# Optimization experiments

Hardware: AMD Instinct MI355X
Metric: run time of the kernel (lower is better)

## Reference

```python
import jax, jax.numpy as jnp
import numpy as np

N_NODES = 100000
N_EDGES = 1600000
D = 32


def setup_inputs() -> dict:
    key = jax.random.key(0)
    k1, k2, k3, k4, k5, k6, k7 = jax.random.split(key, 7)
    x = jax.random.normal(k1, (N_NODES, D), dtype=jnp.float32)
    edge_index = jax.random.randint(k2, (2, N_EDGES), 0, N_NODES, dtype=jnp.int64)
    edge_weight = jax.random.uniform(k3, (N_EDGES,), dtype=jnp.float32)
    s = 1.0 / np.sqrt(D)
    W1 = jax.random.uniform(k4, (D, D), jnp.float32, -s, s)
    b1 = jax.random.uniform(k5, (D,), jnp.float32, -s, s)
    W2 = jax.random.uniform(k6, (D, D), jnp.float32, -s, s)
    b2 = jax.random.uniform(k7, (D,), jnp.float32, -s, s)
    return {"x": x, "edge_index": edge_index, "edge_weight": edge_weight,
            "W1": W1, "b1": b1, "W2": W2, "b2": b2}


def reference(x, edge_index, edge_weight, W1, b1, W2, b2):
    N = x.shape[0]
    src, dst = edge_index[0], edge_index[1]
    # gcn_norm with improved=True: self-loops get fill value 2.0
    loops = jnp.arange(N, dtype=edge_index.dtype)
    src_a = jnp.concatenate([src, loops])
    dst_a = jnp.concatenate([dst, loops])
    w_a = jnp.concatenate([edge_weight, jnp.full((N,), 2.0, x.dtype)])
    deg = jax.ops.segment_sum(w_a, dst_a, num_segments=N)          # [N]
    dinv = jnp.where(deg > 0, jax.lax.rsqrt(deg), 0.0)             # deg^-1/2, inf->0
    norm = dinv[src_a] * w_a * dinv[dst_a]                          # [E+N]

    def gcn_conv(h, W, b):
        h = h @ W                                                   # [N,D] dense transform
        msg = h[src_a] * norm[:, None]                              # gather + normalize [E+N,D]
        return jax.ops.segment_sum(msg, dst_a, num_segments=N) + b  # scatter-add + bias

    h = jax.nn.relu(gcn_conv(x, W1, b1))
    h = jax.nn.relu(gcn_conv(h, W2, b2))
    # F.dropout treated as identity (deterministic inference reference)
    return h
```

## Files before the change

kernel.cpp:

```cpp
#include <hip/hip_runtime.h>

#define D       32
#define BS      256
#define CBLK    500
#define CBLKP   500
#define BSH     7
#define BNODES  128
#define MAXBUCK 1024
#define MAX_EPT 13
#define ECAP    4096
#define POISON_BASE ((int)0xAAAAAAAAu)

__device__ inline unsigned bf16pack2(float a, float b) {
    unsigned ua = __float_as_uint(a);
    unsigned ub = __float_as_uint(b);
    ua = (ua + 0x7FFFu + ((ua >> 16) & 1)) >> 16;
    ub = (ub + 0x7FFFu + ((ub >> 16) & 1)) >> 16;
    return ua | (ub << 16);
}
__device__ inline uint2 bf16pack4(float4 v) {
    return make_uint2(bf16pack2(v.x, v.y), bf16pack2(v.z, v.w));
}
__device__ inline float4 bf16unpack4(uint2 h) {
    return make_float4(__uint_as_float(h.x << 16),
                       __uint_as_float(h.x & 0xFFFF0000u),
                       __uint_as_float(h.y << 16),
                       __uint_as_float(h.y & 0xFFFF0000u));
}

__global__ void k_localsort_gemm(const int* __restrict__ dst, const int* __restrict__ src,
                                 const float* __restrict__ w, int* __restrict__ bc,
                                 int* __restrict__ locoff, int2* __restrict__ staged,
                                 int E, int EPB, int NBUCK, int NBUCKP,
                                 const float* __restrict__ X, const float* __restrict__ Wm,
                                 uint2* __restrict__ H, int n) {
    __shared__ int    bins[MAXBUCK];
    __shared__ int    sscan[BS];
    __shared__ int    carry;
    __shared__ float4 Ws[D * 8];
    int t = threadIdx.x;

    if ((int)blockIdx.x >= CBLK) {
        for (int i = t; i < D * 8; i += BS) Ws[i] = ((const float4*)Wm)[i];
        __syncthreads();
        int gid  = (blockIdx.x - CBLK) * BS + t;
        int node = gid >> 3;
        int q    = gid & 7;
        if (node >= n) return;
        float4 xv  = ((const float4*)X)[node * 8 + q];
        float4 acc = make_float4(0.f, 0.f, 0.f, 0.f);
#pragma unroll
        for (int k = 0; k < D; ++k) {
            float comp = (k & 3) == 0 ? xv.x : (k & 3) == 1 ? xv.y
                       : (k & 3) == 2 ? xv.z : xv.w;
            float  xk = __shfl(comp, k >> 2, 8);
            float4 wr = Ws[k * 8 + q];
            acc.x += xk * wr.x; acc.y += xk * wr.y;
            acc.z += xk * wr.z; acc.w += xk * wr.w;
        }
        H[node * 8 + q] = bf16pack4(acc);
        return;
    }

    int blk = blockIdx.x;
    int beg = blk * EPB;
    int end = min(E, beg + EPB);
    for (int i = t; i < NBUCK; i += BS) bins[i] = 0;
    __syncthreads();

    int stash[MAX_EPT];
#pragma unroll
    for (int i = 0; i < MAX_EPT; ++i) {
        int e = beg + i * BS + t;
        stash[i] = -1;
        if (e < end) {
            int dv = dst[e];
            int b  = dv >> BSH;
            int r  = atomicAdd(&bins[b], 1);
            stash[i] = (b << 19) | ((dv & (BNODES - 1)) << 12) | r;
        }
    }
    __syncthreads();
    for (int i = t; i < NBUCK; i += BS) bc[blk * NBUCKP + i] = bins[i];
    __syncthreads();
    if (t == 0) carry = 0;
    __syncthreads();
    for (int base = 0; base < NBUCK; base += BS) {
        int idx = base + t;
        int v = (idx < NBUCK) ? bins[idx] : 0;
        sscan[t] = v;
        __syncthreads();
        for (int off = 1; off < BS; off <<= 1) {
            int u = (t >= off) ? sscan[t - off] : 0;
            __syncthreads();
            sscan[t] += u;
            __syncthreads();
        }
        if (idx < NBUCK) bins[idx] = carry + sscan[t] - v;
        __syncthreads();
        if (t == 0) carry += sscan[BS - 1];
        __syncthreads();
    }
    for (int i = t; i < NBUCK; i += BS) locoff[blk * NBUCKP + i] = bins[i];
    __syncthreads();

    int2* myslice = staged + (size_t)blk * EPB;
#pragma unroll
    for (int i = 0; i < MAX_EPT; ++i) {
        if (stash[i] >= 0) {
            int e     = beg + i * BS + t;
            int b     = stash[i] >> 19;
            int local = (stash[i] >> 12) & (BNODES - 1);
            int r     = stash[i] & 0xFFF;
            int pos   = bins[b] + r;
            myslice[pos] = make_int2(src[e] | (local << 17), __float_as_int(w[e]));
        }
    }
}

__global__ void k_trans(const int* __restrict__ bc, const int* __restrict__ locoff,
                        int* __restrict__ bcT, int* __restrict__ locoffT,
                        int NBUCK, int NBUCKP) {
    __shared__ int tile[32][33];
    const int* in  = (blockIdx.z == 0) ? bc  : locoff;
    int*       out = (blockIdx.z == 0) ? bcT : locoffT;
    int c0 = blockIdx.x * 32;
    int r0 = blockIdx.y * 32;
    int tx = threadIdx.x & 31, ty = threadIdx.x >> 5;
    for (int dy = ty; dy < 32; dy += 8) {
        int r = r0 + dy, c = c0 + tx;
        tile[dy][tx] = (r < CBLK && c < NBUCK) ? in[r * NBUCKP + c] : 0;
    }
    __syncthreads();
    for (int dy = ty; dy < 32; dy += 8) {
        int c = c0 + dy, r = r0 + tx;
        if (c < NBUCK && r < CBLK) out[c * CBLKP + r] = tile[tx][dy];
    }
}

__global__ void k_btot(const int* __restrict__ bcT, int* __restrict__ btot, int NBUCK) {
    int gid = blockIdx.x * BS + threadIdx.x;
    int b = gid >> 3, c = gid & 7;
    if (b >= NBUCK) return;
    int s = 0;
    for (int k = c; k < CBLK; k += 8) s += bcT[b * CBLKP + k];
    s += __shfl_xor(s, 4, 8);
    s += __shfl_xor(s, 2, 8);
    s += __shfl_xor(s, 1, 8);
    if (c == 0) btot[b] = s;
}

__global__ void k_scanB(const int* __restrict__ asum, int* __restrict__ aex, int m) {
    __shared__ int s[BS];
    __shared__ int carry;
    int t = threadIdx.x;
    if (t == 0) carry = 0;
    __syncthreads();
    for (int base = 0; base < m; base += BS) {
        int i = base + t;
        int v = (i < m) ? asum[i] : 0;
        s[t] = v;
        __syncthreads();
        for (int off = 1; off < BS; off <<= 1) {
            int u = (t >= off) ? s[t - off] : 0;
            __syncthreads();
            s[t] += u;
            __syncthreads();
        }
        if (i < m) aex[i] = carry + s[t] - v;
        __syncthreads();
        if (t == BS - 1) carry += s[BS - 1];
        __syncthreads();
    }
}

__global__ void k_merge(const int* __restrict__ bcT, const int* __restrict__ locoffT,
                        const int* __restrict__ boff, const int2* __restrict__ staged,
                        int2* __restrict__ emeta, int* __restrict__ rowptr,
                        float* __restrict__ dinv, uint2* __restrict__ H,
                        int N, int E, int NBUCK, int EPB) {
    __shared__ int2  ebuf[ECAP];
    __shared__ int   runoff[CBLK];
    __shared__ int   lrun[CBLK];
    __shared__ int   sscan[BS];
    __shared__ int   carry;
    __shared__ int   ihist[BNODES];
    __shared__ float fdeg[BNODES];
    __shared__ int   cursor[BNODES];
    __shared__ float sdinv[BNODES];
    __shared__ int   wsum;
    int b = blockIdx.x, t = threadIdx.x;

    for (int k = t; k < CBLK; k += BS) {
        runoff[k] = bcT[b * CBLKP + k];
        lrun[k]   = locoffT[b * CBLKP + k];
    }
    if (t < BNODES) { ihist[t] = 0; fdeg[t] = 0.0f; }
    if (t == 0) carry = 0;
    __syncthreads();
    for (int base = 0; base < CBLK; base += BS) {
        int idx = base + t;
        int v = (idx < CBLK) ? runoff[idx] : 0;
        sscan[t] = v;
        __syncthreads();
        for (int off = 1; off < BS; off <<= 1) {
            int u = (t >= off) ? sscan[t - off] : 0;
            __syncthreads();
            sscan[t] += u;
            __syncthreads();
        }
        if (idx < CBLK) runoff[idx] = carry + sscan[t] - v;
        __syncthreads();
        if (t == 0) carry += sscan[BS - 1];
        __syncthreads();
    }
    int total  = carry;
    int bstart = boff[b];
    bool fits  = total <= ECAP;

    for (int k = t; k < CBLK; k += BS) {
        int gs = runoff[k];
        int ge = (k + 1 < CBLK) ? runoff[k + 1] : total;
        const int2* run = staged + (size_t)k * EPB + lrun[k];
        for (int j = 0; j < ge - gs; ++j) {
            int2 v = run[j];
            int local = (v.x >> 17) & (BNODES - 1);
            atomicAdd(&ihist[local], 1);
            atomicAdd(&fdeg[local], __int_as_float(v.y));
            if (fits) ebuf[gs + j] = v;
        }
    }
    __syncthreads();
    int v128 = 0, incl = 0;
    if (t < BNODES) {
        v128 = ihist[t];
        incl = v128;
#pragma unroll
        for (int off = 1; off < 64; off <<= 1) {
            int u = __shfl_up(incl, off, 64);
            if ((t & 63) >= off) incl += u;
        }
    }
    if (t == 63) wsum = incl;
    __syncthreads();
    if (t < BNODES) {
        if (t >= 64) incl += wsum;
        int excl = incl - v128;
        int node = b * BNODES + t;
        float di = rsqrtf(2.0f + fdeg[t]);
        if (node < N) {
            rowptr[node] = bstart + excl;
            dinv[node]   = di;
        }
        sdinv[t]  = di;
        cursor[t] = excl;
    }
    if (b == NBUCK - 1 && t == 0) rowptr[N] = E;
    __syncthreads();
    {
        int base_node = b * BNODES;
        for (int i = t; i < BNODES * 8; i += BS) {
            int row  = i >> 3;
            int node = base_node + row;
            if (node < N) {
                float di = sdinv[row];
                size_t off = (size_t)node * 8 + (i & 7);
                float4 f = bf16unpack4(H[off]);
                f.x *= di; f.y *= di; f.z *= di; f.w *= di;
                H[off] = bf16pack4(f);
            }
        }
    }
    __syncthreads();
    for (int k = t; k < CBLK; k += BS) {
        int gs = runoff[k];
        int ge = (k + 1 < CBLK) ? runoff[k + 1] : total;
        const int2* run = staged + (size_t)k * EPB + lrun[k];
        for (int j = 0; j < ge - gs; ++j) {
            int2 v = fits ? ebuf[gs + j] : run[j];
            int local = (v.x >> 17) & (BNODES - 1);
            int r = atomicAdd(&cursor[local], 1);
            emeta[bstart + r] = make_int2(v.x & 0x1FFFF, v.y);
        }
    }
}

template <bool FUSE_GEMM>
__global__ void k_agg(const int* __restrict__ rowptr, const int2* __restrict__ emeta,
                      const uint4* __restrict__ Hs, const float* __restrict__ dinv,
                      const float* __restrict__ b, const float* __restrict__ W2,
                      void* __restrict__ outv, int n) {
    __shared__ float4 Ws[D * 8];
    int tid = threadIdx.x;
    if (FUSE_GEMM) {
        for (int i = tid; i < D * 8; i += BS) Ws[i] = ((const float4*)W2)[i];
        __syncthreads();
    }

    int gid  = blockIdx.x * BS + tid;
    int node = gid >> 2;
    int q    = gid & 3;
    if (node >= n) return;

    float  di  = dinv[node];
    float4 bq0 = ((const float4*)b)[q * 2];
    float4 bq1 = ((const float4*)b)[q * 2 + 1];
    uint4  h0  = Hs[node * 4 + q];
    float4 a0  = bf16unpack4(make_uint2(h0.x, h0.y));
    float4 a1  = bf16unpack4(make_uint2(h0.z, h0.w));
    float4 acc0 = make_float4(2.f * a0.x, 2.f * a0.y, 2.f * a0.z, 2.f * a0.w);
    float4 acc1 = make_float4(2.f * a1.x, 2.f * a1.y, 2.f * a1.z, 2.f * a1.w);

    int beg  = rowptr[node];
    int end  = rowptr[node + 1];
    int full = beg + ((end - beg) & ~7);

    for (int i0 = beg; i0 < full; i0 += 8) {
        int2 em0 = emeta[i0 + q];
        int2 em1 = emeta[i0 + 4 + q];
        float nm0 = __int_as_float(em0.y);
        float nm1 = __int_as_float(em1.y);
#pragma unroll
        for (int j = 0; j < 4; ++j) {
            int   s  = __shfl(em0.x, j, 4);
            float nm = __shfl(nm0, j, 4);
            uint4 hv = Hs[s * 4 + q];
            float4 f0 = bf16unpack4(make_uint2(hv.x, hv.y));
            float4 f1 = bf16unpack4(make_uint2(hv.z, hv.w));
            acc0.x += nm * f0.x; acc0.y += nm * f0.y; acc0.z += nm * f0.z; acc0.w += nm * f0.w;
            acc1.x += nm * f1.x; acc1.y += nm * f1.y; acc1.z += nm * f1.z; acc1.w += nm * f1.w;
        }
#pragma unroll
        for (int j = 0; j < 4; ++j) {
            int   s  = __shfl(em1.x, j, 4);
            float nm = __shfl(nm1, j, 4);
            uint4 hv = Hs[s * 4 + q];
            float4 f0 = bf16unpack4(make_uint2(hv.x, hv.y));
            float4 f1 = bf16unpack4(make_uint2(hv.z, hv.w));
            acc0.x += nm * f0.x; acc0.y += nm * f0.y; acc0.z += nm * f0.z; acc0.w += nm * f0.w;
            acc1.x += nm * f1.x; acc1.y += nm * f1.y; acc1.z += nm * f1.z; acc1.w += nm * f1.w;
        }
    }
    if (full < end) {
        int idx0 = full + q;
        int idx1 = full + 4 + q;
        int2 em0 = (idx0 < end) ? emeta[idx0] : make_int2(0, 0);
        int2 em1 = (idx1 < end) ? emeta[idx1] : make_int2(0, 0);
        float nm0 = (idx0 < end) ? __int_as_float(em0.y) : 0.0f;
        float nm1 = (idx1 < end) ? __int_as_float(em1.y) : 0.0f;
        int rem = end - full;
        int r0 = rem < 4 ? rem : 4;
        for (int j = 0; j < r0; ++j) {
            int   s  = __shfl(em0.x, j, 4);
            float nm = __shfl(nm0, j, 4);
            uint4 hv = Hs[s * 4 + q];
            float4 f0 = bf16unpack4(make_uint2(hv.x, hv.y));
            float4 f1 = bf16unpack4(make_uint2(hv.z, hv.w));
            acc0.x += nm * f0.x; acc0.y += nm * f0.y; acc0.z += nm * f0.z; acc0.w += nm * f0.w;
            acc1.x += nm * f1.x; acc1.y += nm * f1.y; acc1.z += nm * f1.z; acc1.w += nm * f1.w;
        }
        for (int j = 0; j < rem - 4; ++j) {
            int   s  = __shfl(em1.x, j, 4);
            float nm = __shfl(nm1, j, 4);
            uint4 hv = Hs[s * 4 + q];
            float4 f0 = bf16unpack4(make_uint2(hv.x, hv.y));
            float4 f1 = bf16unpack4(make_uint2(hv.z, hv.w));
            acc0.x += nm * f0.x; acc0.y += nm * f0.y; acc0.z += nm * f0.z; acc0.w += nm * f0.w;
            acc1.x += nm * f1.x; acc1.y += nm * f1.y; acc1.z += nm * f1.z; acc1.w += nm * f1.w;
        }
    }
    acc0.x = fmaxf(di * acc0.x + bq0.x, 0.f);
    acc0.y = fmaxf(di * acc0.y + bq0.y, 0.f);
    acc0.z = fmaxf(di * acc0.z + bq0.z, 0.f);
    acc0.w = fmaxf(di * acc0.w + bq0.w, 0.f);
    acc1.x = fmaxf(di * acc1.x + bq1.x, 0.f);
    acc1.y = fmaxf(di * acc1.y + bq1.y, 0.f);
    acc1.z = fmaxf(di * acc1.z + bq1.z, 0.f);
    acc1.w = fmaxf(di * acc1.w + bq1.w, 0.f);

    if (FUSE_GEMM) {
        float4 o0 = make_float4(0.f, 0.f, 0.f, 0.f);
        float4 o1 = make_float4(0.f, 0.f, 0.f, 0.f);
#pragma unroll
        for (int k = 0; k < D; ++k) {
            int sel = k & 7;
            float comp = sel == 0 ? acc0.x : sel == 1 ? acc0.y : sel == 2 ? acc0.z
                       : sel == 3 ? acc0.w : sel == 4 ? acc1.x : sel == 5 ? acc1.y
                       : sel == 6 ? acc1.z : acc1.w;
            float  hk = __shfl(comp, k >> 3, 4);
            float4 w0 = Ws[k * 8 + q * 2];
            float4 w1 = Ws[k * 8 + q * 2 + 1];
            o0.x += hk * w0.x; o0.y += hk * w0.y; o0.z += hk * w0.z; o0.w += hk * w0.w;
            o1.x += hk * w1.x; o1.y += hk * w1.y; o1.z += hk * w1.z; o1.w += hk * w1.w;
        }
        o0.x *= di; o0.y *= di; o0.z *= di; o0.w *= di;
        o1.x *= di; o1.y *= di; o1.z *= di; o1.w *= di;
        ((uint4*)outv)[node * 4 + q] =
            make_uint4(bf16pack2(o0.x, o0.y), bf16pack2(o0.z, o0.w),
                       bf16pack2(o1.x, o1.y), bf16pack2(o1.z, o1.w));
    } else {
        ((float4*)outv)[node * 8 + q * 2]     = acc0;
        ((float4*)outv)[node * 8 + q * 2 + 1] = acc1;
    }
}

__global__ void k_hist_gemm(const int4* __restrict__ dst4, int* __restrict__ cnt,
                            int4* __restrict__ rank4, int E4,
                            const float* __restrict__ X, const float* __restrict__ W,
                            uint2* __restrict__ H, int n, int gE4) {
    __shared__ float4 Ws[D * 8];
    int tid = threadIdx.x;
    if ((int)blockIdx.x < gE4) {
        int i = blockIdx.x * BS + tid;
        if (i >= E4) return;
        int4 d = dst4[i];
        int4 r;
        r.x = atomicAdd(&cnt[d.x], 1) - POISON_BASE;
        r.y = atomicAdd(&cnt[d.y], 1) - POISON_BASE;
        r.z = atomicAdd(&cnt[d.z], 1) - POISON_BASE;
        r.w = atomicAdd(&cnt[d.w], 1) - POISON_BASE;
        rank4[i] = r;
        return;
    }
    for (int i = tid; i < D * 8; i += BS) Ws[i] = ((const float4*)W)[i];
    __syncthreads();
    int gid  = (blockIdx.x - gE4) * BS + tid;
    int node = gid >> 3;
    int q    = gid & 7;
    if (node >= n) return;
    float4 xv  = ((const float4*)X)[node * 8 + q];
    float4 acc = make_float4(0.f, 0.f, 0.f, 0.f);
#pragma unroll
    for (int k = 0; k < D; ++k) {
        float comp = (k & 3) == 0 ? xv.x : (k & 3) == 1 ? xv.y
                   : (k & 3) == 2 ? xv.z : xv.w;
        float  xk = __shfl(comp, k >> 2, 8);
        float4 wr = Ws[k * 8 + q];
        acc.x += xk * wr.x; acc.y += xk * wr.y;
        acc.z += xk * wr.z; acc.w += xk * wr.w;
    }
    H[node * 8 + q] = bf16pack4(acc);
}

__global__ void k_scan1(const int* __restrict__ cnt, int* __restrict__ bsum, int n) {
    __shared__ int s[BS];
    int t = threadIdx.x, i = blockIdx.x * BS + t;
    s[t] = (i < n) ? (cnt[i] - POISON_BASE) : 0;
    __syncthreads();
    for (int off = BS / 2; off > 0; off >>= 1) {
        if (t < off) s[t] += s[t + off];
        __syncthreads();
    }
    if (t == 0) bsum[blockIdx.x] = s[0];
}

__global__ void k_scan23(const int* __restrict__ cnt, const int* __restrict__ bsum,
                         int* __restrict__ rowptr, int n) {
    __shared__ int red[BS];
    __shared__ int s[BS];
    int t = threadIdx.x, i = blockIdx.x * BS + t;
    int pacc = 0;
    for (int k = t; k < (int)blockIdx.x; k += BS) pacc += bsum[k];
    red[t] = pacc;
    __syncthreads();
    for (int off = BS / 2; off > 0; off >>= 1) {
        if (t < off) red[t] += red[t + off];
        __syncthreads();
    }
    int bpre = red[0];
    int v = (i < n) ? (cnt[i] - POISON_BASE) : 0;
    s[t] = v;
    __syncthreads();
    for (int off = 1; off < BS; off <<= 1) {
        int u = (t >= off) ? s[t - off] : 0;
        __syncthreads();
        s[t] += u;
        __syncthreads();
    }
    if (i < n) {
        int excl = bpre + s[t] - v;
        rowptr[i] = excl;
        if (i == n - 1) rowptr[n] = excl + v;
    }
}

__global__ void k_reorder(const int4* __restrict__ src4, const int4* __restrict__ dst4,
                          const float4* __restrict__ w4, const int4* __restrict__ rank4,
                          const int* __restrict__ rowptr, int2* __restrict__ emeta, int E4) {
    int i = blockIdx.x * blockDim.x + threadIdx.x;
    if (i >= E4) return;
    int4   s = src4[i];
    int4   d = dst4[i];
    float4 w = w4[i];
    int4   r = rank4[i];
    emeta[rowptr[d.x] + r.x] = make_int2(s.x, __float_as_int(w.x));
    emeta[rowptr[d.y] + r.y] = make_int2(s.y, __float_as_int(w.y));
    emeta[rowptr[d.z] + r.z] = make_int2(s.z, __float_as_int(w.z));
    emeta[rowptr[d.w] + r.w] = make_int2(s.w, __float_as_int(w.w));
}

__global__ void k_degscaleF(const int* __restrict__ rowptr, const int2* __restrict__ emeta,
                            float* __restrict__ dinv, uint2* __restrict__ H, int n) {
    int gid  = blockIdx.x * blockDim.x + threadIdx.x;
    int node = gid >> 3;
    int c    = gid & 7;
    if (node >= n) return;
    int beg = rowptr[node], end = rowptr[node + 1];
    float sum = 0.0f;
    for (int idx = beg + c; idx < end; idx += 8)
        sum += __int_as_float(emeta[idx].y);
    sum += __shfl_xor(sum, 4, 8);
    sum += __shfl_xor(sum, 2, 8);
    sum += __shfl_xor(sum, 1, 8);
    float di = rsqrtf(2.0f + sum);
    if (c == 0) dinv[node] = di;
    di = __shfl(di, 0, 8);
    size_t off = (size_t)node * 8 + c;
    float4 f = bf16unpack4(H[off]);
    f.x *= di; f.y *= di; f.z *= di; f.w *= di;
    H[off] = bf16pack4(f);
}

extern "C" void kernel_launch(void* const* d_in, const int* in_sizes, int n_in,
                              void* d_out, int out_size, void* d_ws, size_t ws_size,
                              hipStream_t stream) {
    const float* x   = (const float*)d_in[0];
    const int*   ei  = (const int*)d_in[1];
    const float* w   = (const float*)d_in[2];
    const float* W1  = (const float*)d_in[3];
    const float* b1  = (const float*)d_in[4];
    const float* W2  = (const float*)d_in[5];
    const float* b2  = (const float*)d_in[6];
    float*       out = (float*)d_out;

    const int N = in_sizes[0] / D;
    const int E = in_sizes[2];
    const int* src = ei;
    const int* dst = ei + E;

    const int NBUCK  = (N + BNODES - 1) / BNODES;
    const int NBUCKP = (NBUCK + 3) & ~3;
    const int EPB    = (E + CBLK - 1) / CBLK;
    const int NB     = (N + BS - 1) / BS;
    const int E4     = E / 4;
    const int gE4    = (E4 + BS - 1) / BS;
    const int gN8    = (N * 8 + BS - 1) / BS;
    const int gN4    = (N * 4 + BS - 1) / BS;

    char*  base    = (char*)d_ws;
    int2*  emeta   = (int2*)base;
    uint2* ht      = (uint2*)(base + (size_t)E * 8);
    uint2* ht2     = ht + (size_t)N * 8;
    float* dinv    = (float*)(ht2 + (size_t)N * 8);
    int*   rowptr  = (int*)(dinv + N);
    int2*  staged  = (int2*)(rowptr + ((N + 4) & ~3));
    int*   bc      = (int*)(staged + E);
    int*   locoff  = bc + (size_t)CBLK * NBUCKP;
    int*   bcT     = locoff + (size_t)CBLK * NBUCKP;
    int*   locoffT = bcT + (size_t)NBUCK * CBLKP;
    int*   btot    = locoffT + (size_t)NBUCK * CBLKP;
    int*   boff    = btot + NBUCKP;
    size_t need    = (size_t)((char*)(boff + NBUCKP) - base);

    bool main_ok = (ws_size >= need) && (NBUCK <= MAXBUCK) && (N < (1 << 17)) &&
                   ((EPB + BS - 1) / BS <= MAX_EPT) && (EPB <= 4096) && (N % 4 == 0);

    if (main_ok) {
        k_localsort_gemm<<<CBLK + gN8, BS, 0, stream>>>(dst, src, w, bc, locoff, staged,
                                                        E, EPB, NBUCK, NBUCKP, x, W1, ht, N);
        dim3 tg((NBUCK + 31) / 32, (CBLK + 31) / 32, 2);
        k_trans<<<tg, BS, 0, stream>>>(bc, locoff, bcT, locoffT, NBUCK, NBUCKP);
        k_btot <<<(NBUCK * 8 + BS - 1) / BS, BS, 0, stream>>>(bcT, btot, NBUCK);
        k_scanB<<<1, BS, 0, stream>>>(btot, boff, NBUCK);
        k_merge<<<NBUCK, BS, 0, stream>>>(bcT, locoffT, boff, staged, emeta, rowptr, dinv,
                                          ht, N, E, NBUCK, EPB);
        k_agg<true ><<<gN4, BS, 0, stream>>>(rowptr, emeta, (const uint4*)ht,  dinv, b1, W2, ht2, N);
        k_agg<false><<<gN4, BS, 0, stream>>>(rowptr, emeta, (const uint4*)ht2, dinv, b2, nullptr, out, N);
    } else {
        int* cnt  = (int*)staged;
        int* rank = cnt + N;
        int* bsum = rank + E;
        k_hist_gemm<<<gE4 + gN8, BS, 0, stream>>>((const int4*)dst, cnt, (int4*)rank, E4,
                                                  x, W1, ht, N, gE4);
        k_scan1 <<<NB, BS, 0, stream>>>(cnt, bsum, N);
        k_scan23<<<NB, BS, 0, stream>>>(cnt, bsum, rowptr, N);
        k_reorder<<<(E4 + BS - 1) / BS, BS, 0, stream>>>((const int4*)src, (const int4*)dst,
                                                         (const float4*)w, (const int4*)rank,
                                                         rowptr, emeta, E4);
        k_degscaleF<<<gN8, BS, 0, stream>>>(rowptr, emeta, dinv, ht, N);
        k_agg<true ><<<gN4, BS, 0, stream>>>(rowptr, emeta, (const uint4*)ht,  dinv, b1, W2, ht2, N);
        k_agg<false><<<gN4, BS, 0, stream>>>(rowptr, emeta, (const uint4*)ht2, dinv, b2, nullptr, out, N);
    }
}
```

Baseline: 208.5 us.

## Fold bucket totals into transpose, compute offsets in merge, cache edge loads

Bucket totals are now accumulated with atomics inside the transpose kernel. Each merge block computes its own exclusive prefix by reducing the totals of all preceding buckets, which removes two kernel launches (k_btot and the single-block k_scanB). The local sort also loads src and w once into registers during the first pass, so the scatter pass no longer re-reads them from global memory. The cost is a memset launch, redundant O(NBUCK) reductions in every merge block, and more registers per thread in the local sort.

```diff
diff --git a/kernel.cpp b/kernel.cpp
--- a/kernel.cpp
+++ b/kernel.cpp
@@ -68,7 +68,9 @@
     for (int i = t; i < NBUCK; i += BS) bins[i] = 0;
     __syncthreads();
 
-    int stash[MAX_EPT];
+    int   stash[MAX_EPT];
+    int   ssrc[MAX_EPT];
+    float swv[MAX_EPT];
 #pragma unroll
     for (int i = 0; i < MAX_EPT; ++i) {
         int e = beg + i * BS + t;
@@ -77,7 +79,9 @@
             int dv = dst[e];
             int b  = dv >> BSH;
             int r  = atomicAdd(&bins[b], 1);
-            stash[i] = (b << 19) | ((dv & (BNODES - 1)) << 12) | r;
+            stash[i] = (b << 12) | r;
+            ssrc[i]  = src[e] | ((dv & (BNODES - 1)) << 17);
+            swv[i]   = w[e];
         }
     }
     __syncthreads();
@@ -108,19 +112,17 @@
 #pragma unroll
     for (int i = 0; i < MAX_EPT; ++i) {
         if (stash[i] >= 0) {
-            int e     = beg + i * BS + t;
-            int b     = stash[i] >> 19;
-            int local = (stash[i] >> 12) & (BNODES - 1);
-            int r     = stash[i] & 0xFFF;
-            int pos   = bins[b] + r;
-            myslice[pos] = make_int2(src[e] | (local << 17), __float_as_int(w[e]));
+            int b   = stash[i] >> 12;
+            int r   = stash[i] & 0xFFF;
+            int pos = bins[b] + r;
+            myslice[pos] = make_int2(ssrc[i], __float_as_int(swv[i]));
         }
     }
 }
 
 __global__ void k_trans(const int* __restrict__ bc, const int* __restrict__ locoff,
                         int* __restrict__ bcT, int* __restrict__ locoffT,
-                        int NBUCK, int NBUCKP) {
+                        int* __restrict__ btot, int NBUCK, int NBUCKP) {
     __shared__ int tile[32][33];
     const int* in  = (blockIdx.z == 0) ? bc  : locoff;
     int*       out = (blockIdx.z == 0) ? bcT : locoffT;
@@ -136,46 +138,16 @@
         int c = c0 + dy, r = r0 + tx;
         if (c < NBUCK && r < CBLK) out[c * CBLKP + r] = tile[tx][dy];
     }
-}
-
-__global__ void k_btot(const int* __restrict__ bcT, int* __restrict__ btot, int NBUCK) {
-    int gid = blockIdx.x * BS + threadIdx.x;
-    int b = gid >> 3, c = gid & 7;
-    if (b >= NBUCK) return;
-    int s = 0;
-    for (int k = c; k < CBLK; k += 8) s += bcT[b * CBLKP + k];
-    s += __shfl_xor(s, 4, 8);
-    s += __shfl_xor(s, 2, 8);
-    s += __shfl_xor(s, 1, 8);
-    if (c == 0) btot[b] = s;
-}
-
-__global__ void k_scanB(const int* __restrict__ asum, int* __restrict__ aex, int m) {
-    __shared__ int s[BS];
-    __shared__ int carry;
-    int t = threadIdx.x;
-    if (t == 0) carry = 0;
-    __syncthreads();
-    for (int base = 0; base < m; base += BS) {
-        int i = base + t;
-        int v = (i < m) ? asum[i] : 0;
-        s[t] = v;
-        __syncthreads();
-        for (int off = 1; off < BS; off <<= 1) {
-            int u = (t >= off) ? s[t - off] : 0;
-            __syncthreads();
-            s[t] += u;
-            __syncthreads();
-        }
-        if (i < m) aex[i] = carry + s[t] - v;
-        __syncthreads();
-        if (t == BS - 1) carry += s[BS - 1];
-        __syncthreads();
+    if (blockIdx.z == 0 && ty == 0 && c0 + tx < NBUCK) {
+        int s = 0;
+#pragma unroll
+        for (int dy = 0; dy < 32; ++dy) s += tile[dy][tx];
+        if (s) atomicAdd(&btot[c0 + tx], s);
     }
 }
 
 __global__ void k_merge(const int* __restrict__ bcT, const int* __restrict__ locoffT,
-                        const int* __restrict__ boff, const int2* __restrict__ staged,
+                        const int* __restrict__ btot, const int2* __restrict__ staged,
                         int2* __restrict__ emeta, int* __restrict__ rowptr,
                         float* __restrict__ dinv, uint2* __restrict__ H,
                         int N, int E, int NBUCK, int EPB) {
@@ -189,7 +161,22 @@
     __shared__ int   cursor[BNODES];
     __shared__ float sdinv[BNODES];
     __shared__ int   wsum;
+    __shared__ int   bstart_s;
     int b = blockIdx.x, t = threadIdx.x;
+
+    {
+        int pacc = 0;
+        for (int k = t; k < b; k += BS) pacc += btot[k];
+        sscan[t] = pacc;
+        __syncthreads();
+        for (int off = BS / 2; off > 0; off >>= 1) {
+            if (t < off) sscan[t] += sscan[t + off];
+            __syncthreads();
+        }
+        if (t == 0) bstart_s = sscan[0];
+        __syncthreads();
+    }
+    int bstart = bstart_s;
 
     for (int k = t; k < CBLK; k += BS) {
         runoff[k] = bcT[b * CBLKP + k];
@@ -214,9 +201,8 @@
         if (t == 0) carry += sscan[BS - 1];
         __syncthreads();
     }
-    int total  = carry;
-    int bstart = boff[b];
-    bool fits  = total <= ECAP;
+    int total = carry;
+    bool fits = total <= ECAP;
 
     for (int k = t; k < CBLK; k += BS) {
         int gs = runoff[k];
@@ -559,20 +545,18 @@
     int*   bcT     = locoff + (size_t)CBLK * NBUCKP;
     int*   locoffT = bcT + (size_t)NBUCK * CBLKP;
     int*   btot    = locoffT + (size_t)NBUCK * CBLKP;
-    int*   boff    = btot + NBUCKP;
-    size_t need    = (size_t)((char*)(boff + NBUCKP) - base);
+    size_t need    = (size_t)((char*)(btot + NBUCKP) - base);
 
     bool main_ok = (ws_size >= need) && (NBUCK <= MAXBUCK) && (N < (1 << 17)) &&
                    ((EPB + BS - 1) / BS <= MAX_EPT) && (EPB <= 4096) && (N % 4 == 0);
 
     if (main_ok) {
+        hipMemsetAsync(btot, 0, (size_t)NBUCKP * 4, stream);
         k_localsort_gemm<<<CBLK + gN8, BS, 0, stream>>>(dst, src, w, bc, locoff, staged,
                                                         E, EPB, NBUCK, NBUCKP, x, W1, ht, N);
         dim3 tg((NBUCK + 31) / 32, (CBLK + 31) / 32, 2);
-        k_trans<<<tg, BS, 0, stream>>>(bc, locoff, bcT, locoffT, NBUCK, NBUCKP);
-        k_btot <<<(NBUCK * 8 + BS - 1) / BS, BS, 0, stream>>>(bcT, btot, NBUCK);
-        k_scanB<<<1, BS, 0, stream>>>(btot, boff, NBUCK);
-        k_merge<<<NBUCK, BS, 0, stream>>>(bcT, locoffT, boff, staged, emeta, rowptr, dinv,
+        k_trans<<<tg, BS, 0, stream>>>(bc, locoff, bcT, locoffT, btot, NBUCK, NBUCKP);
+        k_merge<<<NBUCK, BS, 0, stream>>>(bcT, locoffT, btot, staged, emeta, rowptr, dinv,
                                           ht, N, E, NBUCK, EPB);
         k_agg<true ><<<gN4, BS, 0, stream>>>(rowptr, emeta, (const uint4*)ht,  dinv, b1, W2, ht2, N);
         k_agg<false><<<gN4, BS, 0, stream>>>(rowptr, emeta, (const uint4*)ht2, dinv, b2, nullptr, out, N);
```

Result: faster. 195.8 us (-6.1%).
